# Kernel tuning notes

Measured on AMD Instinct MI355X. Metric: run time of the kernel, lower is better.

## Reference

```python
import jax, jax.numpy as jnp
import numpy as np

R = 32            # voxel resolution
DIM = 240         # channels C
EPS_NORM = 0.0    # module eps
BN_EPS = 1e-5     # torch BatchNorm1d default eps


def setup_inputs() -> dict:
    key = jax.random.key(0)
    k1, k2, k3 = jax.random.split(key, 3)
    B, C, N = 4, DIM, 32768
    features = jax.random.normal(k1, (B, C, N), jnp.float32)
    coords = jax.random.uniform(k2, (B, 3, N), jnp.float32)
    # mlp params: Conv1d(2C -> C, kernel 1) + BatchNorm1d(C)
    w = jax.random.normal(k3, (C, 2 * C), jnp.float32) / np.sqrt(2 * C).astype(np.float32)
    b = jnp.zeros((C,), jnp.float32)
    gamma = jnp.ones((C,), jnp.float32)
    beta = jnp.zeros((C,), jnp.float32)
    return {"features": features, "coords": coords, "w": w, "b": b, "gamma": gamma, "beta": beta}


def _voxelize(features, coords):
    # normalize coords into [0, 1], scale to voxel grid
    nc = coords - coords.mean(axis=2, keepdims=True)                      # [B,3,N]
    scale = jnp.linalg.norm(nc, axis=1, keepdims=True).max(axis=2, keepdims=True) * 2.0 + EPS_NORM
    nc = nc / scale + 0.5
    nc = jnp.clip(nc * R, 0, R - 1)
    vox = jnp.round(nc).astype(jnp.int32)
    pos = vox[:, 0] + vox[:, 1] * R + vox[:, 2] * (R * R)                 # [B,N] flattened voxel id
    R3 = R * R * R

    def per_batch(f, p):
        # f: [C,N], p: [N] -> [2C, R3]; per-voxel max feature + second (min) feature
        mx = jax.ops.segment_max(f.T, p, num_segments=R3)                 # [R3, C]
        mn = jax.ops.segment_min(f.T, p, num_segments=R3)                 # [R3, C]
        cnt = jax.ops.segment_sum(jnp.ones_like(p), p, num_segments=R3)  # [R3]
        mask = (cnt > 0)[:, None]
        mx = jnp.where(mask, mx, 0.0)
        mn = jnp.where(mask, mn, 0.0)
        return jnp.concatenate([mx, mn], axis=1).T                        # [2C, R3]

    fea = jax.vmap(per_batch)(features, pos)                              # [B,2C,R3]
    return fea, nc


def reference(features, coords, w, b, gamma, beta):
    fea, nc = _voxelize(features, coords)
    # 1x1 Conv1d (pointwise GEMM) + BatchNorm1d (training-mode batch stats) + Swish
    y = jnp.einsum('co,bov->bcv', w, fea) + b[None, :, None]
    mean = y.mean(axis=(0, 2), keepdims=True)
    var = y.var(axis=(0, 2), keepdims=True)
    y = gamma[None, :, None] * (y - mean) * jax.lax.rsqrt(var + BN_EPS) + beta[None, :, None]
    y = y * jax.nn.sigmoid(y)
    B, C, _ = features.shape
    return y.reshape(B, C, R, R, R), nc
```

## Files before the change

kernel.cpp:

```cpp
#include <hip/hip_runtime.h>
#include <cstdint>
#include <cstddef>

#define RR 32
#define R3 32768
#define NPT 32768
#define CH 240
#define CH2 480
#define NB 4
#define NTILES 2048
#define Y_ELEMS 31457280

typedef __attribute__((ext_vector_type(8))) short short8v;
typedef __attribute__((ext_vector_type(4))) float float4v;

union u8pack { short8v v; unsigned short u[8]; };

static __device__ __forceinline__ float bf2f(unsigned short u) {
  return __uint_as_float(((unsigned int)u) << 16);
}
static __device__ __forceinline__ unsigned short f2bf(float f) {
  unsigned int u = __float_as_uint(f);
  u = (u + 0x7FFFu + ((u >> 16) & 1u)) >> 16;
  return (unsigned short)u;
}

__global__ void k_init(int* __restrict__ cnt, float* __restrict__ stats,
                       const float* __restrict__ w, unsigned short* __restrict__ wfrag,
                       int* __restrict__ tilectr) {
  int g = blockIdx.x * 256 + threadIdx.x;
  if (g == 0) *tilectr = 0;
  if (g < NB * R3) cnt[g] = 0;
  if (g < 4096) stats[g] = 0.0f;
  if (g < 14400) {
    int lane = g & 63, t = g >> 6;
    int mg = t / 75, r = t % 75;
    int kc = r / 5, mL = r % 5;
    int m = mg * 5 + mL;
    int ln = lane & 15, q = lane >> 4;
    const float* src = w + (size_t)(m * 16 + ln) * CH2 + kc * 32 + q * 8;
    u8pack pk;
#pragma unroll
    for (int j = 0; j < 8; j++) pk.u[j] = f2bf(src[j]);
    *(short8v*)&wfrag[(size_t)g * 8] = pk.v;
  }
}

__global__ __launch_bounds__(1024) void k_coord_stats(const float* __restrict__ coords,
                                                      float* __restrict__ ms) {
  __shared__ float red[1024];
  __shared__ float mean[3];
  int b = blockIdx.x, t = threadIdx.x;
  const float4* cb4 = (const float4*)(coords + (size_t)b * 3 * NPT);
  float s[3] = {0.f, 0.f, 0.f};
  for (int i = t; i < NPT / 4; i += 1024) {
#pragma unroll
    for (int d = 0; d < 3; d++) {
      float4 v = cb4[d * (NPT / 4) + i];
      s[d] += (v.x + v.y) + (v.z + v.w);
    }
  }
  for (int d = 0; d < 3; d++) {
    red[t] = s[d]; __syncthreads();
    for (int k = 512; k > 0; k >>= 1) { if (t < k) red[t] += red[t + k]; __syncthreads(); }
    if (t == 0) mean[d] = red[0] * (1.0f / NPT);
    __syncthreads();
  }
  float m0 = mean[0], m1 = mean[1], m2 = mean[2];
  float mx = 0.f;
  for (int i = t; i < NPT / 4; i += 1024) {
    float4 x = cb4[i], y = cb4[NPT / 4 + i], z = cb4[2 * (NPT / 4) + i];
    float dx, dy, dz, n;
    dx = x.x - m0; dy = y.x - m1; dz = z.x - m2; n = dx * dx + dy * dy + dz * dz; mx = fmaxf(mx, n);
    dx = x.y - m0; dy = y.y - m1; dz = z.y - m2; n = dx * dx + dy * dy + dz * dz; mx = fmaxf(mx, n);
    dx = x.z - m0; dy = y.z - m1; dz = z.z - m2; n = dx * dx + dy * dy + dz * dz; mx = fmaxf(mx, n);
    dx = x.w - m0; dy = y.w - m1; dz = z.w - m2; n = dx * dx + dy * dy + dz * dz; mx = fmaxf(mx, n);
  }
  red[t] = mx; __syncthreads();
  for (int k = 512; k > 0; k >>= 1) { if (t < k) red[t] = fmaxf(red[t], red[t + k]); __syncthreads(); }
  if (t == 0) {
    ms[b * 4 + 0] = m0; ms[b * 4 + 1] = m1; ms[b * 4 + 2] = m2;
    ms[b * 4 + 3] = sqrtf(red[0]) * 2.0f;
  }
}

__global__ void k_pos_nc(const float* __restrict__ coords, const float* __restrict__ ms,
                         float* __restrict__ ncout, int* __restrict__ pos, int* __restrict__ cnt) {
  int g = blockIdx.x * 256 + threadIdx.x;
  int b = g >> 15, i = g & (NPT - 1);
  const float* cb = coords + (size_t)b * 3 * NPT;
  float scale = ms[b * 4 + 3];
  int vox[3];
#pragma unroll
  for (int d = 0; d < 3; d++) {
    float v = (cb[(size_t)d * NPT + i] - ms[b * 4 + d]) / scale + 0.5f;
    v = fminf(fmaxf(v * (float)RR, 0.0f), (float)(RR - 1));
    ncout[((size_t)(b * 3 + d)) * NPT + i] = v;
    vox[d] = (int)rintf(v);
  }
  int p = (b << 15) | (vox[0] + (vox[1] << 5) + (vox[2] << 10));
  pos[g] = p;
  atomicAdd(&cnt[p], 1);
}

__global__ void k_scan(const int* __restrict__ cnt, int* __restrict__ offs) {
  __shared__ int part[1024];
  int b = blockIdx.x, t = threadIdx.x;
  const int base = b * R3;
  int local[32];
  int s = 0;
#pragma unroll
  for (int j = 0; j < 32; j++) { local[j] = cnt[base + t * 32 + j]; s += local[j]; }
  part[t] = s; __syncthreads();
  for (int d = 1; d < 1024; d <<= 1) {
    int v = (t >= d) ? part[t - d] : 0;
    __syncthreads();
    part[t] += v;
    __syncthreads();
  }
  int run = (t == 0) ? 0 : part[t - 1];
#pragma unroll
  for (int j = 0; j < 32; j++) { offs[base + t * 32 + j] = run; run += local[j]; }
}

__global__ void k_scatter(const int* __restrict__ pos, int* __restrict__ offs,
                          int* __restrict__ rank) {
  int g = blockIdx.x * 256 + threadIdx.x;
  int p = pos[g];
  int slot = atomicAdd(&offs[p], 1);
  rank[g] = slot;
}

__global__ void k_transpose3(const float* __restrict__ f, const int* __restrict__ rank,
                             unsigned short* __restrict__ fts) {
  __shared__ float tile[CH * 65];
  __shared__ int slts[64];
  int p0 = blockIdx.x * 64, b = blockIdx.y;
  int t = threadIdx.x;
  if (t < 64) slts[t] = rank[b * NPT + p0 + t];
  {
    int pp = t & 63, cq = t >> 6;
    const float* src = f + ((size_t)b * CH) * NPT + p0 + pp;
#pragma unroll 4
    for (int j = 0; j < 60; ++j) {
      int c = j * 4 + cq;
      tile[c * 65 + pp] = src[(size_t)c * NPT];
    }
  }
  __syncthreads();
  int ch8 = t & 7;
#pragma unroll
  for (int pass = 0; pass < 2; ++pass) {
    int p = pass * 32 + (t >> 3);
    unsigned short* dst = fts + ((size_t)(b * NPT + slts[p])) * CH;
#pragma unroll
    for (int i = 0; i < 4; ++i) {
      int ch = ch8 + 8 * i;
      if (ch < 30) {
        u8pack pk;
#pragma unroll
        for (int jj = 0; jj < 8; ++jj) pk.u[jj] = f2bf(tile[(ch * 8 + jj) * 65 + p]);
        *(short8v*)&dst[ch * 8] = pk.v;
      }
    }
  }
}

__global__ __launch_bounds__(512, 2) void k_fused(const int* __restrict__ cnt,
                                                  const int* __restrict__ offs,
                                                  const unsigned short* __restrict__ fts,
                                                  const unsigned short* __restrict__ wfrag,
                                                  const float* __restrict__ bias,
                                                  unsigned short* __restrict__ ybf,
                                                  float* __restrict__ gstats,
                                                  int* __restrict__ tilectr) {
  __shared__ unsigned short fB[2][4 * 15 * 512];
  __shared__ int scnt[2][64], soffs[2][64], vlist[2][64];
  __shared__ int qh[2], qm[2], tq[4];
  int tid = threadIdx.x;
  int wave = tid >> 6, lane = tid & 63;
  int sub = lane >> 5, l = lane & 31;
  int ln = lane & 15, q = lane >> 4;

  int nmt = (wave == 7) ? 1 : 2;
  short8v wreg[2][15];
#pragma unroll
  for (int mm = 0; mm < 2; ++mm)
    if (mm < nmt) {
      int mt = wave * 2 + mm;
      int mg = mt / 5, mL = mt % 5;
      const unsigned short* wp = wfrag + ((size_t)(mg * 75 + mL) * 512) + lane * 8;
#pragma unroll
      for (int kc = 0; kc < 15; ++kc)
        wreg[mm][kc] = *(const short8v*)(wp + (size_t)kc * 5 * 512);
    }

  float bb[2][4];
#pragma unroll
  for (int mm = 0; mm < 2; ++mm)
    if (mm < nmt) {
      int mt = wave * 2 + mm;
#pragma unroll
      for (int r = 0; r < 4; ++r) bb[mm][r] = bias[mt * 16 + q * 4 + r];
    }
  float sacc[2][4], sqacc[2][4];
#pragma unroll
  for (int mm = 0; mm < 2; ++mm)
#pragma unroll
    for (int r = 0; r < 4; ++r) { sacc[mm][r] = 0.f; sqacc[mm][r] = 0.f; }

  int t1c = 30 + l;
  int kc0 = l >> 2, q0 = l & 3;
  int kc1 = t1c >> 2, q1 = t1c & 3;

  auto GATHER = [&](int sb, int T) {
    unsigned short* fb = fB[sb];
    int bbase = (T >> 9) << 15;
    int qmL = qm[sb];
    while (true) {
      int p;
      if (l == 0) p = atomicAdd(&qh[sb], 1);
      p = __shfl(p, sub << 5);
      if (p >= qmL) break;
      int lv = vlist[sb][p];
      int n = scnt[sb][lv];
      int start = soffs[sb][lv] - n;
      int cg = lv >> 4, cc = lv & 15;
      if (l < 30) {
        const unsigned short* sp = fts + (size_t)(bbase + start) * CH + l * 8;
        int lim = (n - 1) * CH;
        float mx[8], mn[8];
#pragma unroll
        for (int k = 0; k < 8; k++) { mx[k] = -__builtin_inff(); mn[k] = __builtin_inff(); }
        for (int j = 0; j < n; j += 8) {
          int base = j * CH;
          u8pack u0, u1, u2, u3, u4, u5, u6, u7;
          int o0 = base;           o0 = o0 < lim ? o0 : lim;
          int o1 = base + CH;      o1 = o1 < lim ? o1 : lim;
          int o2 = base + 2 * CH;  o2 = o2 < lim ? o2 : lim;
          int o3 = base + 3 * CH;  o3 = o3 < lim ? o3 : lim;
          int o4 = base + 4 * CH;  o4 = o4 < lim ? o4 : lim;
          int o5 = base + 5 * CH;  o5 = o5 < lim ? o5 : lim;
          int o6 = base + 6 * CH;  o6 = o6 < lim ? o6 : lim;
          int o7 = base + 7 * CH;  o7 = o7 < lim ? o7 : lim;
          u0.v = *(const short8v*)(sp + o0);
          u1.v = *(const short8v*)(sp + o1);
          u2.v = *(const short8v*)(sp + o2);
          u3.v = *(const short8v*)(sp + o3);
          u4.v = *(const short8v*)(sp + o4);
          u5.v = *(const short8v*)(sp + o5);
          u6.v = *(const short8v*)(sp + o6);
          u7.v = *(const short8v*)(sp + o7);
#pragma unroll
          for (int k = 0; k < 8; k++) {
            float a0 = bf2f(u0.u[k]), a1 = bf2f(u1.u[k]);
            float a2 = bf2f(u2.u[k]), a3 = bf2f(u3.u[k]);
            float a4 = bf2f(u4.u[k]), a5 = bf2f(u5.u[k]);
            float a6 = bf2f(u6.u[k]), a7 = bf2f(u7.u[k]);
            float hx = fmaxf(fmaxf(fmaxf(a0, a1), fmaxf(a2, a3)),
                             fmaxf(fmaxf(a4, a5), fmaxf(a6, a7)));
            float hn = fminf(fminf(fminf(a0, a1), fminf(a2, a3)),
                             fminf(fminf(a4, a5), fminf(a6, a7)));
            mx[k] = fmaxf(mx[k], hx);
            mn[k] = fminf(mn[k], hn);
          }
        }
        u8pack omx, omn;
#pragma unroll
        for (int k = 0; k < 8; k++) { omx.u[k] = f2bf(mx[k]); omn.u[k] = f2bf(mn[k]); }
        int ci0 = (q0 * 16 + cc) ^ (kc0 & 7);
        int ci1 = (q1 * 16 + cc) ^ (kc1 & 7);
        *(short8v*)&fb[((cg * 15 + kc0) * 64 + ci0) * 8] = omx.v;
        *(short8v*)&fb[((cg * 15 + kc1) * 64 + ci1) * 8] = omn.v;
      }
    }
  };

  if (wave == 0) {
    int t;
    if (lane == 0) t = atomicAdd(tilectr, 1);
    int T0w = __shfl(t, 0);
    if (lane == 0) t = atomicAdd(tilectr, 1);
    int T1w = __shfl(t, 0);
    if (lane == 0) { tq[0] = T0w; tq[1] = T1w; }
    int na = 0, oa = 0, nb2 = 0, ob = 0;
    if (T0w < NTILES) { na = cnt[T0w * 64 + lane]; oa = offs[T0w * 64 + lane]; }
    if (T1w < NTILES) { nb2 = cnt[T1w * 64 + lane]; ob = offs[T1w * 64 + lane]; }
    scnt[0][lane] = na; soffs[0][lane] = oa;
    {
      unsigned long long m = __ballot(na > 0);
      int pfx = __popcll(m & ((1ull << lane) - 1ull));
      if (na > 0) vlist[0][pfx] = lane;
      if (lane == 0) { qm[0] = __popcll(m); qh[0] = 0; }
    }
    scnt[1][lane] = nb2; soffs[1][lane] = ob;
    {
      unsigned long long m = __ballot(nb2 > 0);
      int pfx = __popcll(m & ((1ull << lane) - 1ull));
      if (nb2 > 0) vlist[1][pfx] = lane;
      if (lane == 0) { qm[1] = __popcll(m); qh[1] = 0; }
    }
  }
  {
    int4 z4 = {0, 0, 0, 0};
    for (int i2 = tid; i2 < 3840; i2 += 512) ((int4*)fB[0])[i2] = z4;
  }
  __syncthreads();
  {
    int T0v = tq[0];
    if (T0v < NTILES) GATHER(0, T0v);
  }

  for (int it = 0;; ++it) {
    __syncthreads();
    int T = tq[it & 3];
    if (T >= NTILES) break;
    int cb = it & 1, nb = cb ^ 1;
    int Tn = tq[(it + 1) & 3];

    {
      int4 z4 = {0, 0, 0, 0};
      for (int i2 = tid; i2 < 3840; i2 += 512) ((int4*)fB[nb])[i2] = z4;
    }
    int n2 = 0, o2 = 0;
    if (wave == 0) {
      int t;
      if (lane == 0) t = atomicAdd(tilectr, 1);
      int Tn2 = __shfl(t, 0);
      if (lane == 0) tq[(it + 2) & 3] = Tn2;
      if (Tn2 < NTILES) { n2 = cnt[Tn2 * 64 + lane]; o2 = offs[Tn2 * 64 + lane]; }
    }
    __syncthreads();

    if (Tn < NTILES) GATHER(nb, Tn);

    float4v acc[2][4];
#pragma unroll
    for (int mm = 0; mm < 2; ++mm)
#pragma unroll
      for (int cg = 0; cg < 4; ++cg) acc[mm][cg] = (float4v){0.f, 0.f, 0.f, 0.f};

    const unsigned short* fbase = fB[cb];
#pragma unroll
    for (int kc = 0; kc < 15; ++kc) {
      const unsigned short* fbl = fbase + (size_t)((lane ^ (kc & 7)) * 8);
      short8v bfv[4];
#pragma unroll
      for (int cg = 0; cg < 4; ++cg)
        bfv[cg] = *(const short8v*)(fbl + (size_t)(cg * 15 + kc) * 512);
#pragma unroll
      for (int mm = 0; mm < 2; ++mm)
        if (mm < nmt)
#pragma unroll
          for (int cg = 0; cg < 4; ++cg)
            acc[mm][cg] = __builtin_amdgcn_mfma_f32_16x16x32_bf16(wreg[mm][kc], bfv[cg], acc[mm][cg], 0, 0, 0);
    }

    int bt = T >> 9;
    int v0 = (T & 511) * 64;
    unsigned short* yb = ybf + ((size_t)bt * CH) * R3 + v0 + ln;
#pragma unroll
    for (int mm = 0; mm < 2; ++mm)
      if (mm < nmt) {
        int mt = wave * 2 + mm;
#pragma unroll
        for (int r = 0; r < 4; ++r) {
          int c = mt * 16 + q * 4 + r;
          unsigned short* yrow = yb + (size_t)c * R3;
          float bbv = bb[mm][r];
          float s = 0.f, sq = 0.f;
#pragma unroll
          for (int cg = 0; cg < 4; ++cg) {
            float yv = acc[mm][cg][r] + bbv;
            yrow[cg * 16] = f2bf(yv);
            s += yv; sq += yv * yv;
          }
          sacc[mm][r] += s;
          sqacc[mm][r] += sq;
        }
      }

    if (wave == 0) {
      int s2 = it & 1;
      scnt[s2][lane] = n2; soffs[s2][lane] = o2;
      unsigned long long m = __ballot(n2 > 0);
      int pfx = __popcll(m & ((1ull << lane) - 1ull));
      if (n2 > 0) vlist[s2][pfx] = lane;
      if (lane == 0) { qm[s2] = __popcll(m); qh[s2] = 0; }
    }
  }

  float* gslot = gstats + (size_t)(blockIdx.x & 7) * 512;
#pragma unroll
  for (int mm = 0; mm < 2; ++mm)
    if (mm < nmt) {
      int mt = wave * 2 + mm;
#pragma unroll
      for (int r = 0; r < 4; ++r) {
        float s = sacc[mm][r], sq = sqacc[mm][r];
#pragma unroll
        for (int off = 1; off < 16; off <<= 1) {
          s += __shfl_xor(s, off);
          sq += __shfl_xor(sq, off);
        }
        if (ln == 0) {
          int c = mt * 16 + q * 4 + r;
          atomicAdd(&gslot[c], s);
          atomicAdd(&gslot[256 + c], sq);
        }
      }
    }
}

__global__ void k_apply(const unsigned short* __restrict__ ybf, float* __restrict__ out,
                        const float* __restrict__ stats, const float* __restrict__ gamma,
                        const float* __restrict__ beta) {
  int g = blockIdx.x * 256 + threadIdx.x;
  int c = (g >> 12) % CH;
  const float ninv = 1.0f / (float)(NB * R3);
  float sum = 0.f, ssq = 0.f;
#pragma unroll
  for (int sl = 0; sl < 8; ++sl) {
    sum += stats[sl * 512 + c];
    ssq += stats[sl * 512 + 256 + c];
  }
  float mean = sum * ninv;
  float var = ssq * ninv - mean * mean;
  float s = gamma[c] * rsqrtf(var + 1e-5f);
  float h = beta[c] - mean * s;
  u8pack v;
  v.v = *(const short8v*)(ybf + (size_t)g * 8);
  float4 o0, o1;
  float t;
  t = bf2f(v.u[0]) * s + h; o0.x = t / (1.0f + __expf(-t));
  t = bf2f(v.u[1]) * s + h; o0.y = t / (1.0f + __expf(-t));
  t = bf2f(v.u[2]) * s + h; o0.z = t / (1.0f + __expf(-t));
  t = bf2f(v.u[3]) * s + h; o0.w = t / (1.0f + __expf(-t));
  t = bf2f(v.u[4]) * s + h; o1.x = t / (1.0f + __expf(-t));
  t = bf2f(v.u[5]) * s + h; o1.y = t / (1.0f + __expf(-t));
  t = bf2f(v.u[6]) * s + h; o1.z = t / (1.0f + __expf(-t));
  t = bf2f(v.u[7]) * s + h; o1.w = t / (1.0f + __expf(-t));
  ((float4*)out)[(size_t)g * 2] = o0;
  ((float4*)out)[(size_t)g * 2 + 1] = o1;
}

extern "C" void kernel_launch(void* const* d_in, const int* in_sizes, int n_in,
                              void* d_out, int out_size, void* d_ws, size_t ws_size,
                              hipStream_t stream) {
  const float* features = (const float*)d_in[0];
  const float* coords   = (const float*)d_in[1];
  const float* w        = (const float*)d_in[2];
  const float* bias     = (const float*)d_in[3];
  const float* gamma    = (const float*)d_in[4];
  const float* beta     = (const float*)d_in[5];
  float* out = (float*)d_out;

  char* ws = (char*)d_ws;
  size_t off = 0;
  float* ms    = (float*)(ws + off); off += 256;
  int* tilectr = (int*)(ws + off);   off += 256;
  float* stats = (float*)(ws + off); off += 16384;
  int* pos     = (int*)(ws + off);   off += (size_t)NB * NPT * 4;
  int* cnt     = (int*)(ws + off);   off += (size_t)NB * R3 * 4;
  int* offs    = (int*)(ws + off);   off += (size_t)NB * R3 * 4;
  int* rank    = (int*)(ws + off);   off += (size_t)NB * NPT * 4;
  unsigned short* wfrag = (unsigned short*)(ws + off); off += (size_t)CH * CH2 * 2;
  unsigned short* fts   = (unsigned short*)(ws + off); off += (size_t)NB * NPT * CH * 2;
  unsigned short* ybf   = (unsigned short*)(ws + off); off += (size_t)NB * R3 * CH * 2;

  float* ncout = out + Y_ELEMS;

  k_init<<<516, 256, 0, stream>>>(cnt, stats, w, wfrag, tilectr);
  k_coord_stats<<<4, 1024, 0, stream>>>(coords, ms);
  k_pos_nc<<<512, 256, 0, stream>>>(coords, ms, ncout, pos, cnt);
  k_scan<<<4, 1024, 0, stream>>>(cnt, offs);
  k_scatter<<<512, 256, 0, stream>>>(pos, offs, rank);
  k_transpose3<<<dim3(512, 4), 256, 0, stream>>>(features, rank, fts);
  k_fused<<<256, 512, 0, stream>>>(cnt, offs, fts, wfrag, bias, ybf, stats, tilectr);
  k_apply<<<Y_ELEMS / 2048, 256, 0, stream>>>(ybf, out, stats, gamma, beta);
}
```

Before: 364.6 us.

## Vectorize transpose loads, zero only empty voxel slots, precompute BN scale/shift

The transpose kernel now loads features as float4, converts to bf16 before staging, and keeps a half-size bf16 shared tile, which allows higher occupancy. The fused kernel no longer clears the whole next gather buffer each tile; it builds a list of empty voxels and writes zeros only into their fragments during the gather. BN mean/variance are reduced once in a new single-block kernel instead of in every thread of the apply kernel. The cost is an extra kernel launch and more complex per-tile bookkeeping in shared memory.

After: 369.6 us. Within noise of the previous version (+1.4%).

```diff
diff --git a/kernel.cpp b/kernel.cpp
--- a/kernel.cpp
+++ b/kernel.cpp
@@ -12,9 +12,11 @@
 #define Y_ELEMS 31457280
 
 typedef __attribute__((ext_vector_type(8))) short short8v;
+typedef __attribute__((ext_vector_type(4))) short short4v;
 typedef __attribute__((ext_vector_type(4))) float float4v;
 
 union u8pack { short8v v; unsigned short u[8]; };
+union u4pack { short4v v; unsigned short u[4]; };
 
 static __device__ __forceinline__ float bf2f(unsigned short u) {
   return __uint_as_float(((unsigned int)u) << 16);
@@ -131,20 +133,24 @@
   rank[g] = slot;
 }
 
-__global__ void k_transpose3(const float* __restrict__ f, const int* __restrict__ rank,
-                             unsigned short* __restrict__ fts) {
-  __shared__ float tile[CH * 65];
+__global__ __launch_bounds__(256, 4) void k_transpose3(const float* __restrict__ f,
+                                                       const int* __restrict__ rank,
+                                                       unsigned short* __restrict__ fts) {
+  __shared__ unsigned short tile[CH * 68];
   __shared__ int slts[64];
   int p0 = blockIdx.x * 64, b = blockIdx.y;
   int t = threadIdx.x;
   if (t < 64) slts[t] = rank[b * NPT + p0 + t];
   {
-    int pp = t & 63, cq = t >> 6;
-    const float* src = f + ((size_t)b * CH) * NPT + p0 + pp;
-#pragma unroll 4
-    for (int j = 0; j < 60; ++j) {
-      int c = j * 4 + cq;
-      tile[c * 65 + pp] = src[(size_t)c * NPT];
+    int pg = t & 15, cq = t >> 4;
+    const float* src = f + ((size_t)b * CH + cq) * NPT + p0 + pg * 4;
+#pragma unroll
+    for (int j = 0; j < 15; ++j) {
+      float4 v = *(const float4*)(src + (size_t)(j * 16) * NPT);
+      int c = j * 16 + cq;
+      u4pack p4;
+      p4.u[0] = f2bf(v.x); p4.u[1] = f2bf(v.y); p4.u[2] = f2bf(v.z); p4.u[3] = f2bf(v.w);
+      *(short4v*)&tile[c * 68 + pg * 4] = p4.v;
     }
   }
   __syncthreads();
@@ -159,7 +165,7 @@
       if (ch < 30) {
         u8pack pk;
 #pragma unroll
-        for (int jj = 0; jj < 8; ++jj) pk.u[jj] = f2bf(tile[(ch * 8 + jj) * 65 + p]);
+        for (int jj = 0; jj < 8; ++jj) pk.u[jj] = tile[(ch * 8 + jj) * 68 + p];
         *(short8v*)&dst[ch * 8] = pk.v;
       }
     }
@@ -175,8 +181,8 @@
                                                   float* __restrict__ gstats,
                                                   int* __restrict__ tilectr) {
   __shared__ unsigned short fB[2][4 * 15 * 512];
-  __shared__ int scnt[2][64], soffs[2][64], vlist[2][64];
-  __shared__ int qh[2], qm[2], tq[4];
+  __shared__ int scnt[2][64], soffs[2][64], vlist[2][64], elist[2][64];
+  __shared__ int qh[2], qm[2], em[2], tq[4];
   int tid = threadIdx.x;
   int wave = tid >> 6, lane = tid & 63;
   int sub = lane >> 5, l = lane & 31;
@@ -212,6 +218,17 @@
   int t1c = 30 + l;
   int kc0 = l >> 2, q0 = l & 3;
   int kc1 = t1c >> 2, q1 = t1c & 3;
+  int proc = wave * 2 + sub;
+
+  auto BUILD = [&](int sb, int n, int off) {
+    scnt[sb][lane] = n; soffs[sb][lane] = off;
+    unsigned long long m = __ballot(n > 0);
+    int pfx = __popcll(m & ((1ull << lane) - 1ull));
+    if (n > 0) vlist[sb][pfx] = lane;
+    int epfx = lane - pfx;
+    if (n == 0) elist[sb][epfx] = lane;
+    if (lane == 0) { qm[sb] = __popcll(m); em[sb] = 64 - __popcll(m); qh[sb] = 0; }
+  };
 
   auto GATHER = [&](int sb, int T) {
     unsigned short* fb = fB[sb];
@@ -274,6 +291,20 @@
         *(short8v*)&fb[((cg * 15 + kc1) * 64 + ci1) * 8] = omn.v;
       }
     }
+    int emL = em[sb];
+    if (l < 30) {
+      u8pack z;
+#pragma unroll
+      for (int k = 0; k < 8; k++) z.u[k] = 0;
+      for (int e = proc; e < emL; e += 16) {
+        int lv = elist[sb][e];
+        int cg = lv >> 4, cc = lv & 15;
+        int ci0 = (q0 * 16 + cc) ^ (kc0 & 7);
+        int ci1 = (q1 * 16 + cc) ^ (kc1 & 7);
+        *(short8v*)&fb[((cg * 15 + kc0) * 64 + ci0) * 8] = z.v;
+        *(short8v*)&fb[((cg * 15 + kc1) * 64 + ci1) * 8] = z.v;
+      }
+    }
   };
 
   if (wave == 0) {
@@ -286,24 +317,8 @@
     int na = 0, oa = 0, nb2 = 0, ob = 0;
     if (T0w < NTILES) { na = cnt[T0w * 64 + lane]; oa = offs[T0w * 64 + lane]; }
     if (T1w < NTILES) { nb2 = cnt[T1w * 64 + lane]; ob = offs[T1w * 64 + lane]; }
-    scnt[0][lane] = na; soffs[0][lane] = oa;
-    {
-      unsigned long long m = __ballot(na > 0);
-      int pfx = __popcll(m & ((1ull << lane) - 1ull));
-      if (na > 0) vlist[0][pfx] = lane;
-      if (lane == 0) { qm[0] = __popcll(m); qh[0] = 0; }
-    }
-    scnt[1][lane] = nb2; soffs[1][lane] = ob;
-    {
-      unsigned long long m = __ballot(nb2 > 0);
-      int pfx = __popcll(m & ((1ull << lane) - 1ull));
-      if (nb2 > 0) vlist[1][pfx] = lane;
-      if (lane == 0) { qm[1] = __popcll(m); qh[1] = 0; }
-    }
-  }
-  {
-    int4 z4 = {0, 0, 0, 0};
-    for (int i2 = tid; i2 < 3840; i2 += 512) ((int4*)fB[0])[i2] = z4;
+    BUILD(0, na, oa);
+    BUILD(1, nb2, ob);
   }
   __syncthreads();
   {
@@ -318,10 +333,6 @@
     int cb = it & 1, nb = cb ^ 1;
     int Tn = tq[(it + 1) & 3];
 
-    {
-      int4 z4 = {0, 0, 0, 0};
-      for (int i2 = tid; i2 < 3840; i2 += 512) ((int4*)fB[nb])[i2] = z4;
-    }
     int n2 = 0, o2 = 0;
     if (wave == 0) {
       int t;
@@ -380,14 +391,7 @@
         }
       }
 
-    if (wave == 0) {
-      int s2 = it & 1;
-      scnt[s2][lane] = n2; soffs[s2][lane] = o2;
-      unsigned long long m = __ballot(n2 > 0);
-      int pfx = __popcll(m & ((1ull << lane) - 1ull));
-      if (n2 > 0) vlist[s2][pfx] = lane;
-      if (lane == 0) { qm[s2] = __popcll(m); qh[s2] = 0; }
-    }
+    if (wave == 0) BUILD(it & 1, n2, o2);
   }
 
   float* gslot = gstats + (size_t)(blockIdx.x & 7) * 512;
@@ -412,22 +416,31 @@
     }
 }
 
+__global__ void k_bnpre(const float* __restrict__ stats, const float* __restrict__ gamma,
+                        const float* __restrict__ beta, float* __restrict__ bnsh) {
+  int c = threadIdx.x;
+  if (c < CH) {
+    const float ninv = 1.0f / (float)(NB * R3);
+    float sum = 0.f, ssq = 0.f;
+#pragma unroll
+    for (int sl = 0; sl < 8; ++sl) {
+      sum += stats[sl * 512 + c];
+      ssq += stats[sl * 512 + 256 + c];
+    }
+    float mean = sum * ninv;
+    float var = ssq * ninv - mean * mean;
+    float s = gamma[c] * rsqrtf(var + 1e-5f);
+    bnsh[c] = s;
+    bnsh[CH + c] = beta[c] - mean * s;
+  }
+}
+
 __global__ void k_apply(const unsigned short* __restrict__ ybf, float* __restrict__ out,
-                        const float* __restrict__ stats, const float* __restrict__ gamma,
-                        const float* __restrict__ beta) {
+                        const float* __restrict__ bnsh) {
   int g = blockIdx.x * 256 + threadIdx.x;
   int c = (g >> 12) % CH;
-  const float ninv = 1.0f / (float)(NB * R3);
-  float sum = 0.f, ssq = 0.f;
-#pragma unroll
-  for (int sl = 0; sl < 8; ++sl) {
-    sum += stats[sl * 512 + c];
-    ssq += stats[sl * 512 + 256 + c];
-  }
-  float mean = sum * ninv;
-  float var = ssq * ninv - mean * mean;
-  float s = gamma[c] * rsqrtf(var + 1e-5f);
-  float h = beta[c] - mean * s;
+  float s = bnsh[c];
+  float h = bnsh[CH + c];
   u8pack v;
   v.v = *(const short8v*)(ybf + (size_t)g * 8);
   float4 o0, o1;
@@ -460,6 +473,7 @@
   float* ms    = (float*)(ws + off); off += 256;
   int* tilectr = (int*)(ws + off);   off += 256;
   float* stats = (float*)(ws + off); off += 16384;
+  float* bnsh  = (float*)(ws + off); off += 2048;
   int* pos     = (int*)(ws + off);   off += (size_t)NB * NPT * 4;
   int* cnt     = (int*)(ws + off);   off += (size_t)NB * R3 * 4;
   int* offs    = (int*)(ws + off);   off += (size_t)NB * R3 * 4;
@@ -477,5 +491,6 @@
   k_scatter<<<512, 256, 0, stream>>>(pos, offs, rank);
   k_transpose3<<<dim3(512, 4), 256, 0, stream>>>(features, rank, fts);
   k_fused<<<256, 512, 0, stream>>>(cnt, offs, fts, wfrag, bias, ybf, stats, tilectr);
-  k_apply<<<Y_ELEMS / 2048, 256, 0, stream>>>(ybf, out, stats, gamma, beta);
-}
+  k_bnpre<<<1, 256, 0, stream>>>(stats, gamma, beta, bnsh);
+  k_apply<<<Y_ELEMS / 2048, 256, 0, stream>>>(ybf, out, bnsh);
+}
```
